# Optimization experiments

Hardware: AMD Instinct MI355X
Metric: run time of the kernel (lower is better)

Reference implementation:

```python
import jax, jax.numpy as jnp
import numpy as np

B, M, N, DQ, H = 4, 4096, 4096, 256, 64

def setup_inputs() -> dict:
    key = jax.random.key(0)
    k1, k2, k3, k4 = jax.random.split(key, 4)
    x = jax.random.normal(k1, (B, M, DQ), dtype=jnp.float32)
    cond = jax.random.normal(k2, (B, N, DQ), dtype=jnp.float32)
    Wq = jax.random.normal(k3, (DQ, H), dtype=jnp.float32) * (1.0 / np.sqrt(DQ))
    Wkv = jax.random.normal(k4, (DQ, 2 * H), dtype=jnp.float32) * (1.0 / np.sqrt(DQ))
    return {"x": x, "cond": cond, "Wq": Wq, "Wkv": Wkv}

def reference(x, cond, Wq, Wkv):
    h = Wq.shape[1]
    q = jnp.einsum('bmi,ih->bmh', x, Wq)          # [B,M,H]
    kv = jnp.einsum('bni,ih->bnh', cond, Wkv)     # [B,N,2H]
    k, v = jnp.split(kv, 2, axis=-1)              # each [B,N,H]
    qk = jnp.einsum('bmd,bnd->bmn', q, k) / jnp.sqrt(jnp.asarray(h, q.dtype))
    attn = jax.nn.softmax(qk, axis=-1)            # [B,M,N]
    out = jnp.einsum('bmn,bnd->bmd', attn, v)     # [B,M,H]
    return out
```

## Files before the change

kernel.cpp:

```cpp
#include <hip/hip_runtime.h>
#include <hip/hip_bf16.h>
#include <cstdint>


#define BB 4
#define MM 4096
#define NN 4096
#define DQm 256
#define DH 64
#define NSP 8
#define NITER (NN / 64 / NSP)
#define QSCALE 0.18033688011112042f

typedef _Float16 half8 __attribute__((ext_vector_type(8)));
typedef _Float16 half4 __attribute__((ext_vector_type(4)));
typedef float floatx16 __attribute__((ext_vector_type(16)));

static __device__ __forceinline__ unsigned pkrtz(float a, float b) {
    union { __fp16 h __attribute__((ext_vector_type(2))); unsigned u; } cv;
    cv.h = __builtin_amdgcn_cvt_pkrtz(a, b);
    return cv.u;
}

static __device__ __forceinline__ void gload16(const void* g, void* l) {
    __builtin_amdgcn_global_load_lds(
        (const __attribute__((address_space(1))) void*)g,
        (__attribute__((address_space(3))) void*)l, 16, 0, 0);
}

__global__ __launch_bounds__(256) void wtrans_kernel(const float* __restrict__ Wq,
                                                     const float* __restrict__ Wkv,
                                                     _Float16* __restrict__ wt) {
    int cout = blockIdx.x;
    int t = threadIdx.x;
    float v = (cout < 64) ? Wq[t * 64 + cout] * QSCALE : Wkv[t * 128 + (cout - 64)];
    _Float16 hi = (_Float16)v;
    _Float16 lo = (_Float16)(v - (float)hi);
    wt[cout * DQm + t] = hi;
    wt[192 * DQm + cout * DQm + t] = lo;
}

__global__ __launch_bounds__(256) void proj_kernel(const float* __restrict__ x,
                                                   const float* __restrict__ cond,
                                                   const _Float16* __restrict__ wt,
                                                   _Float16* __restrict__ q_h,
                                                   _Float16* __restrict__ k_h,
                                                   _Float16* __restrict__ vt_h) {
    __shared__ __align__(16) _Float16 xh[32][264];
    __shared__ __align__(16) _Float16 xl[32][264];
    const int t = threadIdx.x;
    const bool isq = blockIdx.x < (BB * MM / 32);
    const int blk = isq ? blockIdx.x : blockIdx.x - BB * MM / 32;
    const long row0 = (long)blk * 32;
    const float4* xg = (const float4*)((isq ? x : cond) + row0 * DQm);
#pragma unroll
    for (int it = 0; it < 8; ++it) {
        int fid = t + it * 256;
        int row = fid >> 6, c4 = fid & 63;
        float4 v = xg[fid];
        half4 hh = {(_Float16)v.x, (_Float16)v.y, (_Float16)v.z, (_Float16)v.w};
        half4 hl = {(_Float16)(v.x - (float)hh[0]), (_Float16)(v.y - (float)hh[1]),
                    (_Float16)(v.z - (float)hh[2]), (_Float16)(v.w - (float)hh[3])};
        *(half4*)(&xh[row][c4 * 4]) = hh;
        *(half4*)(&xl[row][c4 * 4]) = hl;
    }
    __syncthreads();
    const int lane = t & 63, w = t >> 6, c = lane & 31, h = lane >> 5;
    const _Float16* wlo = wt + 192 * DQm;

    if (isq) {
        const int kh = w & 1, ct = w >> 1;
        floatx16 a1, a2, a3;
#pragma unroll
        for (int i = 0; i < 16; ++i) { a1[i] = 0.f; a2[i] = 0.f; a3[i] = 0.f; }
#pragma unroll
        for (int k8 = 0; k8 < 8; ++k8) {
            int kt = kh * 8 + k8;
            half8 ah = *(const half8*)(&xh[c][kt * 16 + h * 8]);
            half8 al = *(const half8*)(&xl[c][kt * 16 + h * 8]);
            half8 bh = *(const half8*)(wt  + (long)(ct * 32 + c) * DQm + kt * 16 + h * 8);
            half8 bl = *(const half8*)(wlo + (long)(ct * 32 + c) * DQm + kt * 16 + h * 8);
            a1 = __builtin_amdgcn_mfma_f32_32x32x16_f16(ah, bh, a1, 0, 0, 0);
            a2 = __builtin_amdgcn_mfma_f32_32x32x16_f16(ah, bl, a2, 0, 0, 0);
            a3 = __builtin_amdgcn_mfma_f32_32x32x16_f16(al, bh, a3, 0, 0, 0);
        }
        float s[16];
#pragma unroll
        for (int i = 0; i < 16; ++i) s[i] = a1[i] + a2[i] + a3[i];
        float* red = (float*)&xh[0][0];
        __syncthreads();
        if (kh == 1) {
#pragma unroll
            for (int i = 0; i < 16; ++i) red[ct * 1024 + i * 64 + lane] = s[i];
        }
        __syncthreads();
        if (kh == 0) {
#pragma unroll
            for (int i = 0; i < 16; ++i) s[i] += red[ct * 1024 + i * 64 + lane];
#pragma unroll
            for (int r = 0; r < 16; ++r) {
                int m = (r & 3) + 8 * (r >> 2) + 4 * h;
                q_h[(row0 + m) * DH + ct * 32 + c] = (_Float16)s[r];
            }
        }
    } else {
        const int ct = w;
        floatx16 a1, a2, a3;
#pragma unroll
        for (int i = 0; i < 16; ++i) { a1[i] = 0.f; a2[i] = 0.f; a3[i] = 0.f; }
        const long wrow = 64 + ct * 32 + c;
#pragma unroll
        for (int kt = 0; kt < 16; ++kt) {
            half8 ah = *(const half8*)(&xh[c][kt * 16 + h * 8]);
            half8 al = *(const half8*)(&xl[c][kt * 16 + h * 8]);
            half8 bh = *(const half8*)(wt  + wrow * DQm + kt * 16 + h * 8);
            half8 bl = *(const half8*)(wlo + wrow * DQm + kt * 16 + h * 8);
            a1 = __builtin_amdgcn_mfma_f32_32x32x16_f16(ah, bh, a1, 0, 0, 0);
            a2 = __builtin_amdgcn_mfma_f32_32x32x16_f16(ah, bl, a2, 0, 0, 0);
            a3 = __builtin_amdgcn_mfma_f32_32x32x16_f16(al, bh, a3, 0, 0, 0);
        }
        int cout = ct * 32 + c;
        if (cout < 64) {
#pragma unroll
            for (int r = 0; r < 16; ++r) {
                int m = (r & 3) + 8 * (r >> 2) + 4 * h;
                k_h[(row0 + m) * DH + cout] = (_Float16)(a1[r] + a2[r] + a3[r]);
            }
        } else {
            int d = cout - 64;
            long bb = row0 >> 12;
#pragma unroll
            for (int s2 = 0; s2 < 4; ++s2) {
                long n = row0 + 8 * s2 + 4 * h;
                half4 hv;
#pragma unroll
                for (int j = 0; j < 4; ++j)
                    hv[j] = (_Float16)(a1[s2 * 4 + j] + a2[s2 * 4 + j] +
                                       a3[s2 * 4 + j]);
                *(half4*)(vt_h + (bb * DH + d) * NN + (n & 4095)) = hv;
            }
        }
    }
}

__global__ __launch_bounds__(256, 4) void fa_kernel(const _Float16* __restrict__ q_h,
                                                    const _Float16* __restrict__ k_h,
                                                    const _Float16* __restrict__ vt_h,
                                                    float* __restrict__ Opart,
                                                    float2* __restrict__ ml) {
    __shared__ __align__(16) _Float16 k_lds[2][64][64];
    __shared__ __align__(16) _Float16 vt_lds[2][64][64];

    const int t = threadIdx.x;
    const int w = t >> 6;
    const int lane = t & 63;
    const int c = lane & 31;
    const int h = lane >> 5;

    const int bid = blockIdx.x;
    const int sp = bid >> 7;
    const int b  = (bid >> 5) & 3;
    const int mt = bid & 31;
    const int mbase = mt * 128 + w * 32;
    const long qrow = (long)b * MM + mbase + c;

    const int p0 = w * 2048 + (lane << 4);
    const int p1 = p0 + 1024;
    const int q0 = p0 ^ (((p0 >> 7) & 7) << 4);
    const int q1 = p1 ^ (((p1 >> 7) & 7) << 4);
    const int n0f = sp * NITER * 64;
    const char* ks0 = (const char*)k_h + ((long)b * NN + n0f) * DH * 2 + q0;
    const char* ks1 = (const char*)k_h + ((long)b * NN + n0f) * DH * 2 + q1;
    const char* vs0 = (const char*)vt_h +
                      (((long)b * DH + (p0 >> 7)) * NN + n0f) * 2 + (q0 & 127);
    const char* vs1 = (const char*)vt_h +
                      (((long)b * DH + (p1 >> 7)) * NN + n0f) * 2 + (q1 & 127);

#define STAGE(bufi)                                                   \
    do {                                                              \
        char* kld = (char*)(&k_lds[bufi][0][0]) + w * 2048;           \
        char* vld = (char*)(&vt_lds[bufi][0][0]) + w * 2048;          \
        gload16(ks0, kld);                                            \
        gload16(ks1, kld + 1024);                                     \
        gload16(vs0, vld);                                            \
        gload16(vs1, vld + 1024);                                     \
        ks0 += 64 * DH * 2; ks1 += 64 * DH * 2;                       \
        vs0 += 128; vs1 += 128;                                       \
    } while (0)

    const int swb = (c & 7) << 4;
    int koff[4];
#pragma unroll
    for (int kt = 0; kt < 4; ++kt) koff[kt] = (kt * 32 + h * 16) ^ swb;

    half8 qf[4];
#pragma unroll
    for (int kt = 0; kt < 4; ++kt)
        qf[kt] = *(const half8*)(q_h + qrow * DH + kt * 16 + h * 8);

    floatx16 Oc0, Oc1;
#pragma unroll
    for (int i = 0; i < 16; ++i) { Oc0[i] = 0.f; Oc1[i] = 0.f; }
    float m_run = 8.0f, l_run = 0.f;

    STAGE(0);
    __syncthreads();

#pragma unroll 1
    for (int it = 0; it < NITER; ++it) {
        const int pb = it & 1;
        if (it + 1 < NITER) STAGE(pb ^ 1);

        const char* kbase = (const char*)(&k_lds[pb][0][0]);
        const char* vbase = (const char*)(&vt_lds[pb][0][0]);

        floatx16 Sc[2];
        const float negm = -m_run;
        __builtin_amdgcn_s_setprio(1);
#pragma unroll
        for (int a = 0; a < 2; ++a) {
            floatx16 acc;
#pragma unroll
            for (int i = 0; i < 16; ++i) acc[i] = negm;
#pragma unroll
            for (int kt = 0; kt < 4; ++kt) {
                half8 af = *(const half8*)(kbase + (a * 32 + c) * 128 + koff[kt]);
                acc = __builtin_amdgcn_mfma_f32_32x32x16_f16(af, qf[kt], acc, 0, 0, 0);
            }
            Sc[a] = acc;
        }
        __builtin_amdgcn_s_setprio(0);

        float t3[11];
#pragma unroll
        for (int i = 0; i < 10; ++i) {
            float u0 = (3 * i < 16) ? Sc[0][3 * i] : Sc[1][3 * i - 16];
            float u1 = (3 * i + 1 < 16) ? Sc[0][3 * i + 1] : Sc[1][3 * i - 15];
            float u2 = (3 * i + 2 < 16) ? Sc[0][3 * i + 2] : Sc[1][3 * i - 14];
            t3[i] = fmaxf(fmaxf(u0, u1), u2);
        }
        t3[10] = fmaxf(Sc[1][14], Sc[1][15]);
        float m0 = fmaxf(fmaxf(t3[0], t3[1]), t3[2]);
        float m1 = fmaxf(fmaxf(t3[3], t3[4]), t3[5]);
        float m2 = fmaxf(fmaxf(t3[6], t3[7]), t3[8]);
        float lmax = fmaxf(fmaxf(m0, m1), fmaxf(m2, fmaxf(t3[9], t3[10])));
        if (__any(lmax > 8.0f)) {
            float tt = fmaxf(lmax, __shfl_xor(lmax, 32, 64));
            float alpha = exp2f(-tt);
            l_run *= alpha;
#pragma unroll
            for (int i = 0; i < 16; ++i) { Oc0[i] *= alpha; Oc1[i] *= alpha; }
#pragma unroll
            for (int a = 0; a < 2; ++a)
#pragma unroll
                for (int r = 0; r < 16; ++r) Sc[a][r] -= tt;
            m_run += tt;
        }
#pragma unroll
        for (int a = 0; a < 2; ++a)
#pragma unroll
            for (int r = 0; r < 16; ++r) Sc[a][r] = exp2f(Sc[a][r]);

        {
            float ts[16];
#pragma unroll
            for (int i = 0; i < 16; ++i) ts[i] = Sc[0][i] + Sc[1][i];
#pragma unroll
            for (int i = 0; i < 8; ++i) ts[i] += ts[i + 8];
#pragma unroll
            for (int i = 0; i < 4; ++i) ts[i] += ts[i + 4];
            ts[0] += ts[2]; ts[1] += ts[3];
            float tsum = ts[0] + ts[1];
            tsum += __shfl_xor(tsum, 32, 64);
            l_run += tsum;
        }

#pragma unroll
        for (int a = 0; a < 2; ++a) {
            uint2 pk0 = {pkrtz(Sc[a][0],  Sc[a][1]),  pkrtz(Sc[a][2],  Sc[a][3])};
            uint2 pk1 = {pkrtz(Sc[a][4],  Sc[a][5]),  pkrtz(Sc[a][6],  Sc[a][7])};
            uint2 pk2 = {pkrtz(Sc[a][8],  Sc[a][9]),  pkrtz(Sc[a][10], Sc[a][11])};
            uint2 pk3 = {pkrtz(Sc[a][12], Sc[a][13]), pkrtz(Sc[a][14], Sc[a][15])};
            union { uint4 u; half8 f; } f0, f1;
#if __has_builtin(__builtin_amdgcn_permlane32_swap)
            {
                auto r0s = __builtin_amdgcn_permlane32_swap(pk0.x, pk1.x, false, false);
                auto r1s = __builtin_amdgcn_permlane32_swap(pk0.y, pk1.y, false, false);
                auto r2s = __builtin_amdgcn_permlane32_swap(pk2.x, pk3.x, false, false);
                auto r3s = __builtin_amdgcn_permlane32_swap(pk2.y, pk3.y, false, false);
                f0.u.x = r0s[0]; f0.u.z = r0s[1];
                f0.u.y = r1s[0]; f0.u.w = r1s[1];
                f1.u.x = r2s[0]; f1.u.z = r2s[1];
                f1.u.y = r3s[0]; f1.u.w = r3s[1];
            }
#else
            {
                uint2 s0, s1, ex0, ex1;
                s0.x = h ? pk0.x : pk1.x;  s0.y = h ? pk0.y : pk1.y;
                s1.x = h ? pk2.x : pk3.x;  s1.y = h ? pk2.y : pk3.y;
                ex0.x = __shfl_xor((int)s0.x, 32, 64);
                ex0.y = __shfl_xor((int)s0.y, 32, 64);
                ex1.x = __shfl_xor((int)s1.x, 32, 64);
                ex1.y = __shfl_xor((int)s1.y, 32, 64);
                f0.u.x = h ? ex0.x : pk0.x;  f0.u.y = h ? ex0.y : pk0.y;
                f0.u.z = h ? pk1.x : ex0.x;  f0.u.w = h ? pk1.y : ex0.y;
                f1.u.x = h ? ex1.x : pk2.x;  f1.u.y = h ? ex1.y : pk2.y;
                f1.u.z = h ? pk3.x : ex1.x;  f1.u.w = h ? pk3.y : ex1.y;
            }
#endif
            __builtin_amdgcn_s_setprio(1);
#pragma unroll
            for (int bq = 0; bq < 2; ++bq) {
                int kt = 2 * a + bq;
                half8 pf = bq ? f1.f : f0.f;
                half8 vf0 = *(const half8*)(vbase + c * 128 + koff[kt]);
                half8 vf1 = *(const half8*)(vbase + (32 + c) * 128 + koff[kt]);
                Oc0 = __builtin_amdgcn_mfma_f32_32x32x16_f16(vf0, pf, Oc0, 0, 0, 0);
                Oc1 = __builtin_amdgcn_mfma_f32_32x32x16_f16(vf1, pf, Oc1, 0, 0, 0);
            }
            __builtin_amdgcn_s_setprio(0);
        }

        __syncthreads();
    }
#undef STAGE

    const long obase = ((long)sp * BB * MM + (long)b * MM + mbase + c) * DH;
#pragma unroll
    for (int dt = 0; dt < 2; ++dt) {
        const floatx16& O = dt ? Oc1 : Oc0;
#pragma unroll
        for (int s2 = 0; s2 < 4; ++s2) {
            float4 v;
            v.x = O[s2 * 4 + 0]; v.y = O[s2 * 4 + 1];
            v.z = O[s2 * 4 + 2]; v.w = O[s2 * 4 + 3];
            *(float4*)(Opart + obase + dt * 32 + s2 * 8 + h * 4) = v;
        }
    }
    if (h == 0)
        ml[((long)sp * BB + b) * MM + mbase + c] = make_float2(m_run, l_run);
}

__global__ __launch_bounds__(256) void merge_kernel(const float* __restrict__ Opart,
                                                    const float2* __restrict__ ml,
                                                    float* __restrict__ out) {
    const long g4 = (long)blockIdx.x * 256 + threadIdx.x;
    const long row = g4 >> 4;
    float2 p[NSP];
    float mmax = -INFINITY;
#pragma unroll
    for (int i = 0; i < NSP; ++i) {
        p[i] = ml[(long)i * BB * MM + row];
        mmax = fmaxf(mmax, p[i].x);
    }
    float denom = 0.f;
    float4 o = make_float4(0.f, 0.f, 0.f, 0.f);
    const float4* Op4 = (const float4*)Opart;
#pragma unroll
    for (int i = 0; i < NSP; ++i) {
        float ai = exp2f(p[i].x - mmax);
        denom += ai * p[i].y;
        float4 v = Op4[(long)i * (BB * MM * DH / 4) + g4];
        o.x += ai * v.x; o.y += ai * v.y; o.z += ai * v.z; o.w += ai * v.w;
    }
    float inv = 1.0f / denom;
    o.x *= inv; o.y *= inv; o.z *= inv; o.w *= inv;
    ((float4*)out)[g4] = o;
}

extern "C" void kernel_launch(void* const* d_in, const int* in_sizes, int n_in,
                              void* d_out, int out_size, void* d_ws, size_t ws_size,
                              hipStream_t stream) {
    const float* x    = (const float*)d_in[0];
    const float* cond = (const float*)d_in[1];
    const float* Wq   = (const float*)d_in[2];
    const float* Wkv  = (const float*)d_in[3];
    float* out = (float*)d_out;

    char* ws = (char*)d_ws;
    _Float16* wt   = (_Float16*)(ws);
    _Float16* q_h  = (_Float16*)(ws + 196608);
    _Float16* k_h  = (_Float16*)(ws + 196608 + 2097152);
    _Float16* vt_h = (_Float16*)(ws + 196608 + 2 * 2097152);
    float*    Op   = (float*)(ws + 196608 + 3 * 2097152);
    float2*   mlp  = (float2*)(ws + 196608 + 3 * 2097152 + (size_t)NSP * 4194304);

    wtrans_kernel<<<192, 256, 0, stream>>>(Wq, Wkv, wt);
    proj_kernel<<<BB * (MM + NN) / 32, 256, 0, stream>>>(x, cond, wt, q_h, k_h, vt_h);
    fa_kernel<<<NSP * BB * 32, 256, 0, stream>>>(q_h, k_h, vt_h, Op, mlp);
    merge_kernel<<<BB * MM * DH / 4 / 256, 256, 0, stream>>>(Op, mlp, out);
}
```

Baseline: 131.0 us.

## Store normalized split-K partials in fp16 and defer row-sum reduction

The attention kernel now normalizes each split's partial output by its local row sum and stores it as fp16 instead of fp32, halving the partial-output write and the merge kernel's read traffic. The merge kernel weights each split by exp(m)*l and reads 8 halves per thread. The per-iteration row-sum reduction and cross-lane shuffle are replaced by four per-lane accumulators that are reduced once after the loop, and this work is moved after the PV MFMAs. The cost is a small loss of precision in the intermediate partials.

```diff
diff --git a/kernel.cpp b/kernel.cpp
--- a/kernel.cpp
+++ b/kernel.cpp
@@ -146,7 +146,7 @@
 __global__ __launch_bounds__(256, 4) void fa_kernel(const _Float16* __restrict__ q_h,
                                                     const _Float16* __restrict__ k_h,
                                                     const _Float16* __restrict__ vt_h,
-                                                    float* __restrict__ Opart,
+                                                    _Float16* __restrict__ Opart,
                                                     float2* __restrict__ ml) {
     __shared__ __align__(16) _Float16 k_lds[2][64][64];
     __shared__ __align__(16) _Float16 vt_lds[2][64][64];
@@ -201,7 +201,8 @@
     floatx16 Oc0, Oc1;
 #pragma unroll
     for (int i = 0; i < 16; ++i) { Oc0[i] = 0.f; Oc1[i] = 0.f; }
-    float m_run = 8.0f, l_run = 0.f;
+    float l4[4] = {0.f, 0.f, 0.f, 0.f};
+    float m_run = 8.0f;
 
     STAGE(0);
     __syncthreads();
@@ -247,7 +248,8 @@
         if (__any(lmax > 8.0f)) {
             float tt = fmaxf(lmax, __shfl_xor(lmax, 32, 64));
             float alpha = exp2f(-tt);
-            l_run *= alpha;
+#pragma unroll
+            for (int j = 0; j < 4; ++j) l4[j] *= alpha;
 #pragma unroll
             for (int i = 0; i < 16; ++i) { Oc0[i] *= alpha; Oc1[i] *= alpha; }
 #pragma unroll
@@ -260,20 +262,6 @@
         for (int a = 0; a < 2; ++a)
 #pragma unroll
             for (int r = 0; r < 16; ++r) Sc[a][r] = exp2f(Sc[a][r]);
-
-        {
-            float ts[16];
-#pragma unroll
-            for (int i = 0; i < 16; ++i) ts[i] = Sc[0][i] + Sc[1][i];
-#pragma unroll
-            for (int i = 0; i < 8; ++i) ts[i] += ts[i + 8];
-#pragma unroll
-            for (int i = 0; i < 4; ++i) ts[i] += ts[i + 4];
-            ts[0] += ts[2]; ts[1] += ts[3];
-            float tsum = ts[0] + ts[1];
-            tsum += __shfl_xor(tsum, 32, 64);
-            l_run += tsum;
-        }
 
 #pragma unroll
         for (int a = 0; a < 2; ++a) {
@@ -321,31 +309,43 @@
             __builtin_amdgcn_s_setprio(0);
         }
 
+        {
+            float t16v[8];
+#pragma unroll
+            for (int i = 0; i < 8; ++i)
+                t16v[i] = (Sc[0][i] + Sc[0][i + 8]) + (Sc[1][i] + Sc[1][i + 8]);
+#pragma unroll
+            for (int j = 0; j < 4; ++j) l4[j] += t16v[j] + t16v[j + 4];
+        }
+
         __syncthreads();
     }
 #undef STAGE
 
+    float lsum = (l4[0] + l4[1]) + (l4[2] + l4[3]);
+    lsum += __shfl_xor(lsum, 32, 64);
+    const float inv = 1.0f / lsum;
     const long obase = ((long)sp * BB * MM + (long)b * MM + mbase + c) * DH;
 #pragma unroll
     for (int dt = 0; dt < 2; ++dt) {
         const floatx16& O = dt ? Oc1 : Oc0;
 #pragma unroll
         for (int s2 = 0; s2 < 4; ++s2) {
-            float4 v;
-            v.x = O[s2 * 4 + 0]; v.y = O[s2 * 4 + 1];
-            v.z = O[s2 * 4 + 2]; v.w = O[s2 * 4 + 3];
-            *(float4*)(Opart + obase + dt * 32 + s2 * 8 + h * 4) = v;
+            uint2 hv;
+            hv.x = pkrtz(O[s2 * 4 + 0] * inv, O[s2 * 4 + 1] * inv);
+            hv.y = pkrtz(O[s2 * 4 + 2] * inv, O[s2 * 4 + 3] * inv);
+            *(uint2*)(Opart + obase + dt * 32 + s2 * 8 + h * 4) = hv;
         }
     }
     if (h == 0)
-        ml[((long)sp * BB + b) * MM + mbase + c] = make_float2(m_run, l_run);
-}
-
-__global__ __launch_bounds__(256) void merge_kernel(const float* __restrict__ Opart,
+        ml[((long)sp * BB + b) * MM + mbase + c] = make_float2(m_run, lsum);
+}
+
+__global__ __launch_bounds__(256) void merge_kernel(const _Float16* __restrict__ Opart,
                                                     const float2* __restrict__ ml,
                                                     float* __restrict__ out) {
-    const long g4 = (long)blockIdx.x * 256 + threadIdx.x;
-    const long row = g4 >> 4;
+    const long g8 = (long)blockIdx.x * 256 + threadIdx.x;
+    const long row = g8 >> 3;
     float2 p[NSP];
     float mmax = -INFINITY;
 #pragma unroll
@@ -354,18 +354,20 @@
         mmax = fmaxf(mmax, p[i].x);
     }
     float denom = 0.f;
-    float4 o = make_float4(0.f, 0.f, 0.f, 0.f);
-    const float4* Op4 = (const float4*)Opart;
+    float o[8] = {0.f, 0.f, 0.f, 0.f, 0.f, 0.f, 0.f, 0.f};
 #pragma unroll
     for (int i = 0; i < NSP; ++i) {
-        float ai = exp2f(p[i].x - mmax);
-        denom += ai * p[i].y;
-        float4 v = Op4[(long)i * (BB * MM * DH / 4) + g4];
-        o.x += ai * v.x; o.y += ai * v.y; o.z += ai * v.z; o.w += ai * v.w;
+        float wi = exp2f(p[i].x - mmax) * p[i].y;
+        denom += wi;
+        half8 v = *(const half8*)(Opart + (long)i * (BB * MM * DH) + g8 * 8);
+#pragma unroll
+        for (int j = 0; j < 8; ++j) o[j] += wi * (float)v[j];
     }
     float inv = 1.0f / denom;
-    o.x *= inv; o.y *= inv; o.z *= inv; o.w *= inv;
-    ((float4*)out)[g4] = o;
+    float4 o0 = {o[0] * inv, o[1] * inv, o[2] * inv, o[3] * inv};
+    float4 o1 = {o[4] * inv, o[5] * inv, o[6] * inv, o[7] * inv};
+    ((float4*)out)[g8 * 2] = o0;
+    ((float4*)out)[g8 * 2 + 1] = o1;
 }
 
 extern "C" void kernel_launch(void* const* d_in, const int* in_sizes, int n_in,
@@ -382,11 +384,11 @@
     _Float16* q_h  = (_Float16*)(ws + 196608);
     _Float16* k_h  = (_Float16*)(ws + 196608 + 2097152);
     _Float16* vt_h = (_Float16*)(ws + 196608 + 2 * 2097152);
-    float*    Op   = (float*)(ws + 196608 + 3 * 2097152);
-    float2*   mlp  = (float2*)(ws + 196608 + 3 * 2097152 + (size_t)NSP * 4194304);
+    _Float16* Op   = (_Float16*)(ws + 196608 + 3 * 2097152);
+    float2*   mlp  = (float2*)(ws + 196608 + 3 * 2097152 + (size_t)NSP * 2097152);
 
     wtrans_kernel<<<192, 256, 0, stream>>>(Wq, Wkv, wt);
     proj_kernel<<<BB * (MM + NN) / 32, 256, 0, stream>>>(x, cond, wt, q_h, k_h, vt_h);
     fa_kernel<<<NSP * BB * 32, 256, 0, stream>>>(q_h, k_h, vt_h, Op, mlp);
-    merge_kernel<<<BB * MM * DH / 4 / 256, 256, 0, stream>>>(Op, mlp, out);
-}
+    merge_kernel<<<BB * MM * DH / 8 / 256, 256, 0, stream>>>(Op, mlp, out);
+}
```

Measured after the change: 128.4 us, median of 3. -2.0%, faster.
